# Optimization experiments

Hardware: AMD Instinct MI355X
Metric: run time of the kernel (lower is better)

The kernel has to match this reference:

```python
import jax, jax.numpy as jnp
import numpy as np

HEADS = 16


def setup_inputs() -> dict:
    key = jax.random.key(0)
    ks = jax.random.split(key, 6)
    B, S, D = 2, 2048, 1024
    return {
        "x": jax.random.normal(ks[0], (B, S, D), dtype=jnp.float32),
        "q_in": jax.random.normal(ks[1], (B, S, D), dtype=jnp.float32),
        "WQ": jax.random.normal(ks[2], (D, D), dtype=jnp.float32) * 0.03,
        "WK": jax.random.normal(ks[3], (D, D), dtype=jnp.float32) * 0.03,
        "WV": jax.random.normal(ks[4], (D, D), dtype=jnp.float32) * 0.03,
        "WO": jax.random.normal(ks[5], (D, D), dtype=jnp.float32) * 0.03,
    }


def reference(x, q_in, WQ, WK, WV, WO):
    B, S, D = x.shape
    H = HEADS
    hd = D // H
    # projections; tf.split on last dim == reshape to (B,S,H,hd)
    Q = (q_in @ WQ).reshape(B, S, H, hd)
    K = (x @ WK).reshape(B, S, H, hd)
    V = (x @ WV).reshape(B, S, H, hd)
    scores = jnp.einsum("bqhd,bkhd->bhqk", Q, K)  # [B,H,S,S]
    # causal additive mask: 0 on/below diagonal, -inf above
    causal = jnp.tril(jnp.ones((S, S), dtype=bool))
    mask = jnp.where(causal, 0.0, -jnp.inf).astype(scores.dtype)
    # NOTE: original adds the mask BEFORE scaling, and scales by sqrt(d_model)
    attn = jax.nn.softmax((scores + mask) / np.sqrt(D).astype(scores.dtype), axis=-1)
    ctx = jnp.einsum("bhqk,bkhd->bqhd", attn, V).reshape(B, S, D)
    return ctx @ WO
```

## Files before the change

kernel.cpp:

```cpp
#include <hip/hip_runtime.h>


typedef __bf16 bf16_t;
typedef __attribute__((ext_vector_type(8))) __bf16 bf16x8;
typedef __attribute__((ext_vector_type(4))) __bf16 bf16x4;
typedef __attribute__((ext_vector_type(4))) float f32x4;

#define SCALE_LOG2E 0.045084220027780106f
#define FIXED_MAX 8.0f

__device__ __forceinline__ void async_load16(const void* g, void* l) {
  __builtin_amdgcn_global_load_lds(
      (const __attribute__((address_space(1))) void*)g,
      (__attribute__((address_space(3))) void*)l, 16, 0, 0);
}

__global__ void prep(const float* __restrict__ x, const float* __restrict__ q,
                     const float* __restrict__ w0, const float* __restrict__ w1,
                     const float* __restrict__ w2, const float* __restrict__ w3,
                     bf16_t* __restrict__ xb, bf16_t* __restrict__ qb,
                     bf16_t* __restrict__ wt) {
  const int bid = blockIdx.x;
  if (bid < 4096) {
    const float* src = (bid >= 2048) ? q : x;
    bf16_t* dst = (bid >= 2048) ? qb : xb;
    const size_t i = ((size_t)(bid & 2047) * 256 + threadIdx.x) * 8;
    float4 v0 = *(const float4*)(src + i);
    float4 v1 = *(const float4*)(src + i + 4);
    bf16x8 o;
    o[0] = (bf16_t)v0.x; o[1] = (bf16_t)v0.y; o[2] = (bf16_t)v0.z; o[3] = (bf16_t)v0.w;
    o[4] = (bf16_t)v1.x; o[5] = (bf16_t)v1.y; o[6] = (bf16_t)v1.z; o[7] = (bf16_t)v1.w;
    *(bf16x8*)(dst + i) = o;
  } else {
    const int wb = bid - 4096;
    const int z = wb >> 8;
    const float* W = z == 0 ? w0 : z == 1 ? w1 : z == 2 ? w2 : w3;
    bf16_t* dst = wt + (size_t)z * 1048576;
    const int r0 = ((wb >> 4) & 15) * 64, c0 = (wb & 15) * 64;
    __shared__ bf16_t t[64][72];
#pragma unroll
    for (int i = 0; i < 16; ++i) {
      int flat = i * 256 + threadIdx.x;
      int r = flat >> 6, c = flat & 63;
      t[c][r] = (bf16_t)W[(size_t)(r0 + r) * 1024 + c0 + c];
    }
    __syncthreads();
    const int c = threadIdx.x >> 2, seg = (threadIdx.x & 3) * 16;
    bf16x8 a = *(const bf16x8*)&t[c][seg];
    bf16x8 b = *(const bf16x8*)&t[c][seg + 8];
    bf16_t* drow = dst + (size_t)(c0 + c) * 1024 + r0 + seg;
    *(bf16x8*)drow = a;
    *(bf16x8*)(drow + 8) = b;
  }
}

template <int MODE>
__global__ __launch_bounds__(256, MODE == 2 ? 4 : 2) void gemm128(
    const bf16_t* __restrict__ Aq, const bf16_t* __restrict__ Ax,
    const bf16_t* __restrict__ Bt,
    bf16_t* __restrict__ Cq, bf16_t* __restrict__ Cvt, float* __restrict__ Cf) {
  constexpr int K = 1024;
  constexpr int NT = (MODE == 2) ? 2 : 4;
  constexpr int NROWS = NT * 32;
  const int n0 = blockIdx.x * NROWS;
  const int m0 = blockIdx.y * 128;
  const bf16_t* A = (MODE == 0 && n0 >= 1024) ? Ax : Aq;

  __shared__ bf16_t lA[128 * 32];
  __shared__ bf16_t lB[NROWS * 32];

  const int tid = threadIdx.x;
  const int w = tid >> 6, l = tid & 63;
  const int wm = (w & 1) * 64, wn = (w >> 1) * (NT * 16);
  const int sr = l >> 2;
  const int sk = (l & 3) * 8;
  const int fr = l & 15, fc = (l >> 4) * 8;

  f32x4 acc[4][NT] = {};

  for (int kt = 0; kt < K; kt += 32) {
    __syncthreads();
#pragma unroll
    for (int c = 0; c < 2; ++c) {
      const int ch = w * 2 + c;
      async_load16(A + (size_t)(m0 + ch * 16 + sr) * K + kt + sk, &lA[ch * 512]);
      if (NT == 4 || c == 0) {
        const int bch = (NT == 4) ? ch : w;
        async_load16(Bt + (size_t)(n0 + bch * 16 + sr) * K + kt + sk, &lB[bch * 512]);
      }
    }
    __syncthreads();
    bf16x8 af[4], bfr[NT];
#pragma unroll
    for (int i = 0; i < 4; ++i) af[i] = *(const bf16x8*)&lA[(wm + i * 16 + fr) * 32 + fc];
#pragma unroll
    for (int j = 0; j < NT; ++j) bfr[j] = *(const bf16x8*)&lB[(wn + j * 16 + fr) * 32 + fc];
#pragma unroll
    for (int i = 0; i < 4; ++i)
#pragma unroll
      for (int j = 0; j < NT; ++j)
        acc[i][j] = __builtin_amdgcn_mfma_f32_16x16x32_bf16(af[i], bfr[j], acc[i][j], 0, 0, 0);
  }

  if (MODE == 2) {
#pragma unroll
    for (int i = 0; i < 4; ++i) {
      const int m = m0 + wm + i * 16 + (l >> 4) * 4;
#pragma unroll
      for (int j = 0; j < NT; ++j) {
        const int n = n0 + wn + j * 16 + fr;
#pragma unroll
        for (int r = 0; r < 4; ++r) Cf[(size_t)(m + r) * 1024 + n] = acc[i][j][r];
      }
    }
  } else if (n0 < 2048) {
#pragma unroll
    for (int i = 0; i < 4; ++i) {
      const int m = m0 + wm + i * 16 + (l >> 4) * 4;
#pragma unroll
      for (int j = 0; j < NT; ++j) {
        const int n = n0 + wn + j * 16 + fr;
#pragma unroll
        for (int r = 0; r < 4; ++r) Cq[(size_t)(m + r) * 3072 + n] = (bf16_t)acc[i][j][r];
      }
    }
  } else {
#pragma unroll
    for (int i = 0; i < 4; ++i) {
      const int mb = m0 + wm + i * 16 + (l >> 4) * 4;
      const int bb = mb >> 11, ss = mb & 2047;
#pragma unroll
      for (int j = 0; j < NT; ++j) {
        const int nn = n0 - 2048 + wn + j * 16 + fr;
        const int hh = nn >> 6, dd = nn & 63;
        bf16x4 pk;
#pragma unroll
        for (int r = 0; r < 4; ++r) pk[r] = (bf16_t)acc[i][j][r];
        *(bf16x4*)(Cvt + (size_t)((bb * 16 + hh) * 64 + dd) * 2048 + ss) = pk;
      }
    }
  }
}

__global__ __launch_bounds__(256, 2) void attn128(const bf16_t* __restrict__ qkv,
                                                  const bf16_t* __restrict__ vt,
                                                  bf16_t* __restrict__ ctx) {
  const int y = blockIdx.y;
  const int qt = (y < 8) ? (15 - y) : (y - 8);
  const int bh = blockIdx.x;
  const int b = bh >> 4, h = bh & 15;
  const int tid = threadIdx.x, w = tid >> 6, l = tid & 63;
  const int fr = l & 15, fq = l >> 4;

  __shared__ __align__(16) bf16_t lK[2][64 * 64];
  __shared__ __align__(16) bf16_t lV[2][64 * 64];
  __shared__ __align__(16) bf16_t lP[4][32 * 72];

  const int q0 = qt * 128 + w * 32;

  bf16x8 qf[2][2];
#pragma unroll
  for (int u = 0; u < 2; ++u)
#pragma unroll
    for (int ks = 0; ks < 2; ++ks)
      qf[u][ks] = *(const bf16x8*)(qkv + (size_t)(b * 2048 + q0 + u * 16 + fr) * 3072 +
                                   h * 64 + ks * 32 + fq * 8);

  bf16x8 ones;
#pragma unroll
  for (int i = 0; i < 8; ++i) ones[i] = (bf16_t)1.0f;

  f32x4 o[2][4] = {};
  f32x4 liacc[2] = {};

  const int srow = l >> 3;
  const int swz = ((l & 7) ^ srow) * 8;
  const int xr = fr & 7;

  const int ktmax = 2 * qt + 1;
  const bf16_t* kg = qkv + (size_t)b * 2048 * 3072 + 1024 + h * 64;
  const bf16_t* vg = vt + (size_t)(b * 16 + h) * 64 * 2048;

#pragma unroll
  for (int c = 0; c < 2; ++c) {
    const int row = w * 16 + c * 8 + srow;
    async_load16(kg + (size_t)row * 3072 + swz, &lK[0][(w * 16 + c * 8) * 64]);
    async_load16(vg + (size_t)row * 2048 + swz, &lV[0][(w * 16 + c * 8) * 64]);
  }

  for (int kt = 0; kt <= ktmax; ++kt) {
    const int buf = kt & 1;
    __syncthreads();
    if (kt < ktmax) {
#pragma unroll
      for (int c = 0; c < 2; ++c) {
        const int row = w * 16 + c * 8 + srow;
        async_load16(kg + (size_t)((kt + 1) * 64 + row) * 3072 + swz,
                     &lK[buf ^ 1][(w * 16 + c * 8) * 64]);
        async_load16(vg + (size_t)row * 2048 + (kt + 1) * 64 + swz,
                     &lV[buf ^ 1][(w * 16 + c * 8) * 64]);
      }
    }

    const int kbase = kt * 64;
    if (kbase > q0 + 31) continue;

    f32x4 s[2][4] = {};
#pragma unroll
    for (int t = 0; t < 4; ++t)
#pragma unroll
      for (int ks = 0; ks < 2; ++ks) {
        bf16x8 kf = *(const bf16x8*)&lK[buf][(t * 16 + fr) * 64 + ((ks * 4 + fq) ^ xr) * 8];
        s[0][t] = __builtin_amdgcn_mfma_f32_16x16x32_bf16(kf, qf[0][ks], s[0][t], 0, 0, 0);
        s[1][t] = __builtin_amdgcn_mfma_f32_16x16x32_bf16(kf, qf[1][ks], s[1][t], 0, 0, 0);
      }

#pragma unroll
    for (int u = 0; u < 2; ++u) {
      const int qq = q0 + u * 16 + fr;
      const bool needmask = (kbase + 63) > (q0 + u * 16);
#pragma unroll
      for (int t = 0; t < 4; ++t) {
        bf16x4 pk;
#pragma unroll
        for (int r = 0; r < 4; ++r) {
          float v = fmaf(s[u][t][r], SCALE_LOG2E, -FIXED_MAX);
          if (needmask && (kbase + t * 16 + fq * 4 + r > qq)) v = -1e30f;
          pk[r] = (bf16_t)__builtin_amdgcn_exp2f(v);
        }
        *(bf16x4*)&lP[w][(u * 16 + fr) * 72 + t * 16 + fq * 4] = pk;
      }
    }

    bf16x8 pf[2][2];
#pragma unroll
    for (int u = 0; u < 2; ++u)
#pragma unroll
      for (int g = 0; g < 2; ++g)
        pf[u][g] = *(const bf16x8*)&lP[w][(u * 16 + fr) * 72 + g * 32 + fq * 8];
#pragma unroll
    for (int g = 0; g < 2; ++g) {
#pragma unroll
      for (int dt = 0; dt < 4; ++dt) {
        bf16x8 vf = *(const bf16x8*)&lV[buf][(dt * 16 + fr) * 64 + ((g * 4 + fq) ^ xr) * 8];
        o[0][dt] = __builtin_amdgcn_mfma_f32_16x16x32_bf16(vf, pf[0][g], o[0][dt], 0, 0, 0);
        o[1][dt] = __builtin_amdgcn_mfma_f32_16x16x32_bf16(vf, pf[1][g], o[1][dt], 0, 0, 0);
      }
      liacc[0] = __builtin_amdgcn_mfma_f32_16x16x32_bf16(ones, pf[0][g], liacc[0], 0, 0, 0);
      liacc[1] = __builtin_amdgcn_mfma_f32_16x16x32_bf16(ones, pf[1][g], liacc[1], 0, 0, 0);
    }
  }

#pragma unroll
  for (int u = 0; u < 2; ++u) {
    const float inv = 1.f / liacc[u][0];
    bf16_t* cb = ctx + (size_t)(b * 2048 + q0 + u * 16 + fr) * 1024 + h * 64;
#pragma unroll
    for (int dt = 0; dt < 4; ++dt) {
      bf16x4 ov;
#pragma unroll
      for (int r = 0; r < 4; ++r) ov[r] = (bf16_t)(o[u][dt][r] * inv);
      *(bf16x4*)(cb + dt * 16 + fq * 4) = ov;
    }
  }
}

extern "C" void kernel_launch(void* const* d_in, const int* in_sizes, int n_in,
                              void* d_out, int out_size, void* d_ws, size_t ws_size,
                              hipStream_t stream) {
  const float* x  = (const float*)d_in[0];
  const float* q  = (const float*)d_in[1];
  const float* WQ = (const float*)d_in[2];
  const float* WK = (const float*)d_in[3];
  const float* WV = (const float*)d_in[4];
  const float* WO = (const float*)d_in[5];
  float* out = (float*)d_out;

  bf16_t* qb  = (bf16_t*)d_ws;
  bf16_t* xb  = qb + 4194304;
  bf16_t* wt  = xb + 4194304;
  bf16_t* qkv = wt + 4194304;
  bf16_t* vtp = qkv + (size_t)4096 * 3072;
  bf16_t* ctx = vtp + 4194304;

  prep<<<dim3(5120), 256, 0, stream>>>(x, q, WQ, WK, WV, WO, xb, qb, wt);
  gemm128<0><<<dim3(24, 32), 256, 0, stream>>>(qb, xb, wt, qkv, vtp, nullptr);
  attn128<<<dim3(32, 16), 256, 0, stream>>>(qkv, vtp, ctx);
  gemm128<2><<<dim3(16, 32), 256, 0, stream>>>(ctx, ctx, wt + (size_t)3072 * 1024,
                                               nullptr, nullptr, out);
}
```

Measured before the change: 200.6 us.

## Pair complementary 64-row query tiles per block for balanced causal attention

Each attention block now processes two 64-row query tiles in sequence, one late (16+p) and one early (15-p), so every block does roughly the same total causal work. Before, each block handled a single 128-row tile, reordered to launch heavy tiles first. Each wave now holds 16 query rows instead of 32, which lowers register pressure but halves MFMA reuse of each K/V fragment loaded from LDS. K/V tiles are reloaded for the second phase, and the per-kt skip check is removed.

```diff
diff --git a/kernel.cpp b/kernel.cpp
--- a/kernel.cpp
+++ b/kernel.cpp
@@ -142,11 +142,10 @@
   }
 }
 
-__global__ __launch_bounds__(256, 2) void attn128(const bf16_t* __restrict__ qkv,
+__global__ __launch_bounds__(256, 2) void attn64p(const bf16_t* __restrict__ qkv,
                                                   const bf16_t* __restrict__ vt,
                                                   bf16_t* __restrict__ ctx) {
-  const int y = blockIdx.y;
-  const int qt = (y < 8) ? (15 - y) : (y - 8);
+  const int p = blockIdx.y;
   const int bh = blockIdx.x;
   const int b = bh >> 4, h = bh & 15;
   const int tid = threadIdx.x, w = tid >> 6, l = tid & 63;
@@ -154,112 +153,103 @@
 
   __shared__ __align__(16) bf16_t lK[2][64 * 64];
   __shared__ __align__(16) bf16_t lV[2][64 * 64];
-  __shared__ __align__(16) bf16_t lP[4][32 * 72];
-
-  const int q0 = qt * 128 + w * 32;
-
-  bf16x8 qf[2][2];
-#pragma unroll
-  for (int u = 0; u < 2; ++u)
-#pragma unroll
-    for (int ks = 0; ks < 2; ++ks)
-      qf[u][ks] = *(const bf16x8*)(qkv + (size_t)(b * 2048 + q0 + u * 16 + fr) * 3072 +
-                                   h * 64 + ks * 32 + fq * 8);
-
-  bf16x8 ones;
-#pragma unroll
-  for (int i = 0; i < 8; ++i) ones[i] = (bf16_t)1.0f;
-
-  f32x4 o[2][4] = {};
-  f32x4 liacc[2] = {};
+  __shared__ __align__(16) bf16_t lP[4][16 * 72];
+
+  const bf16_t* kg = qkv + (size_t)b * 2048 * 3072 + 1024 + h * 64;
+  const bf16_t* vg = vt + (size_t)(b * 16 + h) * 64 * 2048;
 
   const int srow = l >> 3;
   const int swz = ((l & 7) ^ srow) * 8;
   const int xr = fr & 7;
 
-  const int ktmax = 2 * qt + 1;
-  const bf16_t* kg = qkv + (size_t)b * 2048 * 3072 + 1024 + h * 64;
-  const bf16_t* vg = vt + (size_t)(b * 16 + h) * 64 * 2048;
-
-#pragma unroll
-  for (int c = 0; c < 2; ++c) {
-    const int row = w * 16 + c * 8 + srow;
-    async_load16(kg + (size_t)row * 3072 + swz, &lK[0][(w * 16 + c * 8) * 64]);
-    async_load16(vg + (size_t)row * 2048 + swz, &lV[0][(w * 16 + c * 8) * 64]);
-  }
-
-  for (int kt = 0; kt <= ktmax; ++kt) {
-    const int buf = kt & 1;
-    __syncthreads();
-    if (kt < ktmax) {
-#pragma unroll
-      for (int c = 0; c < 2; ++c) {
-        const int row = w * 16 + c * 8 + srow;
-        async_load16(kg + (size_t)((kt + 1) * 64 + row) * 3072 + swz,
-                     &lK[buf ^ 1][(w * 16 + c * 8) * 64]);
-        async_load16(vg + (size_t)row * 2048 + (kt + 1) * 64 + swz,
-                     &lV[buf ^ 1][(w * 16 + c * 8) * 64]);
-      }
-    }
-
-    const int kbase = kt * 64;
-    if (kbase > q0 + 31) continue;
-
-    f32x4 s[2][4] = {};
-#pragma unroll
-    for (int t = 0; t < 4; ++t)
-#pragma unroll
-      for (int ks = 0; ks < 2; ++ks) {
-        bf16x8 kf = *(const bf16x8*)&lK[buf][(t * 16 + fr) * 64 + ((ks * 4 + fq) ^ xr) * 8];
-        s[0][t] = __builtin_amdgcn_mfma_f32_16x16x32_bf16(kf, qf[0][ks], s[0][t], 0, 0, 0);
-        s[1][t] = __builtin_amdgcn_mfma_f32_16x16x32_bf16(kf, qf[1][ks], s[1][t], 0, 0, 0);
-      }
-
-#pragma unroll
-    for (int u = 0; u < 2; ++u) {
-      const int qq = q0 + u * 16 + fr;
-      const bool needmask = (kbase + 63) > (q0 + u * 16);
+  bf16x8 ones;
+#pragma unroll
+  for (int i = 0; i < 8; ++i) ones[i] = (bf16_t)1.0f;
+
+#pragma unroll 1
+  for (int phase = 0; phase < 2; ++phase) {
+    const int qt = (phase == 0) ? (16 + p) : (15 - p);
+    const int q0 = qt * 64;
+    const int qw = q0 + w * 16;
+    const int ktmax = qt;
+
+    bf16x8 qf[2];
+#pragma unroll
+    for (int ks = 0; ks < 2; ++ks)
+      qf[ks] = *(const bf16x8*)(qkv + (size_t)(b * 2048 + qw + fr) * 3072 +
+                                h * 64 + ks * 32 + fq * 8);
+
+    f32x4 o[4] = {};
+    f32x4 liacc = {};
+
+    if (phase == 1) __syncthreads();
+#pragma unroll
+    for (int c = 0; c < 2; ++c) {
+      const int row = w * 16 + c * 8 + srow;
+      async_load16(kg + (size_t)row * 3072 + swz, &lK[0][(w * 16 + c * 8) * 64]);
+      async_load16(vg + (size_t)row * 2048 + swz, &lV[0][(w * 16 + c * 8) * 64]);
+    }
+
+    for (int kt = 0; kt <= ktmax; ++kt) {
+      const int buf = kt & 1;
+      __syncthreads();
+      if (kt < ktmax) {
+#pragma unroll
+        for (int c = 0; c < 2; ++c) {
+          const int row = w * 16 + c * 8 + srow;
+          async_load16(kg + (size_t)((kt + 1) * 64 + row) * 3072 + swz,
+                       &lK[buf ^ 1][(w * 16 + c * 8) * 64]);
+          async_load16(vg + (size_t)row * 2048 + (kt + 1) * 64 + swz,
+                       &lV[buf ^ 1][(w * 16 + c * 8) * 64]);
+        }
+      }
+
+      f32x4 s[4] = {};
+#pragma unroll
+      for (int t = 0; t < 4; ++t)
+#pragma unroll
+        for (int ks = 0; ks < 2; ++ks) {
+          bf16x8 kf = *(const bf16x8*)&lK[buf][(t * 16 + fr) * 64 + ((ks * 4 + fq) ^ xr) * 8];
+          s[t] = __builtin_amdgcn_mfma_f32_16x16x32_bf16(kf, qf[ks], s[t], 0, 0, 0);
+        }
+
+      const int kbase = kt * 64;
+      const int qq = qw + fr;
+      const bool needmask = (kbase + 63) > qw;
 #pragma unroll
       for (int t = 0; t < 4; ++t) {
         bf16x4 pk;
 #pragma unroll
         for (int r = 0; r < 4; ++r) {
-          float v = fmaf(s[u][t][r], SCALE_LOG2E, -FIXED_MAX);
+          float v = fmaf(s[t][r], SCALE_LOG2E, -FIXED_MAX);
           if (needmask && (kbase + t * 16 + fq * 4 + r > qq)) v = -1e30f;
           pk[r] = (bf16_t)__builtin_amdgcn_exp2f(v);
         }
-        *(bf16x4*)&lP[w][(u * 16 + fr) * 72 + t * 16 + fq * 4] = pk;
-      }
-    }
-
-    bf16x8 pf[2][2];
-#pragma unroll
-    for (int u = 0; u < 2; ++u)
+        *(bf16x4*)&lP[w][fr * 72 + t * 16 + fq * 4] = pk;
+      }
+
+      bf16x8 pf[2];
 #pragma unroll
       for (int g = 0; g < 2; ++g)
-        pf[u][g] = *(const bf16x8*)&lP[w][(u * 16 + fr) * 72 + g * 32 + fq * 8];
-#pragma unroll
-    for (int g = 0; g < 2; ++g) {
-#pragma unroll
-      for (int dt = 0; dt < 4; ++dt) {
-        bf16x8 vf = *(const bf16x8*)&lV[buf][(dt * 16 + fr) * 64 + ((g * 4 + fq) ^ xr) * 8];
-        o[0][dt] = __builtin_amdgcn_mfma_f32_16x16x32_bf16(vf, pf[0][g], o[0][dt], 0, 0, 0);
-        o[1][dt] = __builtin_amdgcn_mfma_f32_16x16x32_bf16(vf, pf[1][g], o[1][dt], 0, 0, 0);
-      }
-      liacc[0] = __builtin_amdgcn_mfma_f32_16x16x32_bf16(ones, pf[0][g], liacc[0], 0, 0, 0);
-      liacc[1] = __builtin_amdgcn_mfma_f32_16x16x32_bf16(ones, pf[1][g], liacc[1], 0, 0, 0);
-    }
-  }
-
-#pragma unroll
-  for (int u = 0; u < 2; ++u) {
-    const float inv = 1.f / liacc[u][0];
-    bf16_t* cb = ctx + (size_t)(b * 2048 + q0 + u * 16 + fr) * 1024 + h * 64;
+        pf[g] = *(const bf16x8*)&lP[w][fr * 72 + g * 32 + fq * 8];
+#pragma unroll
+      for (int g = 0; g < 2; ++g) {
+#pragma unroll
+        for (int dt = 0; dt < 4; ++dt) {
+          bf16x8 vf = *(const bf16x8*)&lV[buf][(dt * 16 + fr) * 64 + ((g * 4 + fq) ^ xr) * 8];
+          o[dt] = __builtin_amdgcn_mfma_f32_16x16x32_bf16(vf, pf[g], o[dt], 0, 0, 0);
+        }
+        liacc = __builtin_amdgcn_mfma_f32_16x16x32_bf16(ones, pf[g], liacc, 0, 0, 0);
+      }
+    }
+
+    const float inv = 1.f / liacc[0];
+    bf16_t* cb = ctx + (size_t)(b * 2048 + qw + fr) * 1024 + h * 64;
 #pragma unroll
     for (int dt = 0; dt < 4; ++dt) {
       bf16x4 ov;
 #pragma unroll
-      for (int r = 0; r < 4; ++r) ov[r] = (bf16_t)(o[u][dt][r] * inv);
+      for (int r = 0; r < 4; ++r) ov[r] = (bf16_t)(o[dt][r] * inv);
       *(bf16x4*)(cb + dt * 16 + fq * 4) = ov;
     }
   }
@@ -285,7 +275,7 @@
 
   prep<<<dim3(5120), 256, 0, stream>>>(x, q, WQ, WK, WV, WO, xb, qb, wt);
   gemm128<0><<<dim3(24, 32), 256, 0, stream>>>(qb, xb, wt, qkv, vtp, nullptr);
-  attn128<<<dim3(32, 16), 256, 0, stream>>>(qkv, vtp, ctx);
+  attn64p<<<dim3(32, 16), 256, 0, stream>>>(qkv, vtp, ctx);
   gemm128<2><<<dim3(16, 32), 256, 0, stream>>>(ctx, ctx, wt + (size_t)3072 * 1024,
                                                nullptr, nullptr, out);
 }
```

Result: faster. 193.6 us (-3.5%).

## Split attention key tiles across wave pairs and pair causal query tiles per block

Applied to the files above, without the earlier changes.

Each block now processes two 64-row query tiles in sequence (tile 16+p, then tile 15-p), so every block does the same amount of causal work. Within a tile, the four waves split into two query halves and two key halves. Each wave handles 32 keys per step, and the two key halves are combined through an LDS reduction before the output is written. The aim is to balance causal load across blocks and reduce the per-wave key work, at the cost of extra syncs, added LDS for the reduction, and reloading K/V for the second phase.

```diff
diff --git a/kernel.cpp b/kernel.cpp
--- a/kernel.cpp
+++ b/kernel.cpp
@@ -142,125 +142,145 @@
   }
 }
 
-__global__ __launch_bounds__(256, 2) void attn128(const bf16_t* __restrict__ qkv,
+__global__ __launch_bounds__(256, 2) void attn64k(const bf16_t* __restrict__ qkv,
                                                   const bf16_t* __restrict__ vt,
                                                   bf16_t* __restrict__ ctx) {
-  const int y = blockIdx.y;
-  const int qt = (y < 8) ? (15 - y) : (y - 8);
+  const int p = blockIdx.y;
   const int bh = blockIdx.x;
   const int b = bh >> 4, h = bh & 15;
   const int tid = threadIdx.x, w = tid >> 6, l = tid & 63;
   const int fr = l & 15, fq = l >> 4;
+  const int qhalf = w & 1, khalf = w >> 1;
 
   __shared__ __align__(16) bf16_t lK[2][64 * 64];
   __shared__ __align__(16) bf16_t lV[2][64 * 64];
-  __shared__ __align__(16) bf16_t lP[4][32 * 72];
-
-  const int q0 = qt * 128 + w * 32;
-
-  bf16x8 qf[2][2];
-#pragma unroll
-  for (int u = 0; u < 2; ++u)
-#pragma unroll
-    for (int ks = 0; ks < 2; ++ks)
-      qf[u][ks] = *(const bf16x8*)(qkv + (size_t)(b * 2048 + q0 + u * 16 + fr) * 3072 +
-                                   h * 64 + ks * 32 + fq * 8);
-
-  bf16x8 ones;
-#pragma unroll
-  for (int i = 0; i < 8; ++i) ones[i] = (bf16_t)1.0f;
-
-  f32x4 o[2][4] = {};
-  f32x4 liacc[2] = {};
+  __shared__ __align__(16) bf16_t lP[4][32 * 32];
+  __shared__ __align__(16) float lRed[2][32][68];
+
+  const bf16_t* kg = qkv + (size_t)b * 2048 * 3072 + 1024 + h * 64;
+  const bf16_t* vg = vt + (size_t)(b * 16 + h) * 64 * 2048;
 
   const int srow = l >> 3;
   const int swz = ((l & 7) ^ srow) * 8;
   const int xr = fr & 7;
-
-  const int ktmax = 2 * qt + 1;
-  const bf16_t* kg = qkv + (size_t)b * 2048 * 3072 + 1024 + h * 64;
-  const bf16_t* vg = vt + (size_t)(b * 16 + h) * 64 * 2048;
-
-#pragma unroll
-  for (int c = 0; c < 2; ++c) {
-    const int row = w * 16 + c * 8 + srow;
-    async_load16(kg + (size_t)row * 3072 + swz, &lK[0][(w * 16 + c * 8) * 64]);
-    async_load16(vg + (size_t)row * 2048 + swz, &lV[0][(w * 16 + c * 8) * 64]);
-  }
-
-  for (int kt = 0; kt <= ktmax; ++kt) {
-    const int buf = kt & 1;
-    __syncthreads();
-    if (kt < ktmax) {
-#pragma unroll
-      for (int c = 0; c < 2; ++c) {
-        const int row = w * 16 + c * 8 + srow;
-        async_load16(kg + (size_t)((kt + 1) * 64 + row) * 3072 + swz,
-                     &lK[buf ^ 1][(w * 16 + c * 8) * 64]);
-        async_load16(vg + (size_t)row * 2048 + (kt + 1) * 64 + swz,
-                     &lV[buf ^ 1][(w * 16 + c * 8) * 64]);
-      }
-    }
-
-    const int kbase = kt * 64;
-    if (kbase > q0 + 31) continue;
-
-    f32x4 s[2][4] = {};
-#pragma unroll
-    for (int t = 0; t < 4; ++t)
-#pragma unroll
-      for (int ks = 0; ks < 2; ++ks) {
-        bf16x8 kf = *(const bf16x8*)&lK[buf][(t * 16 + fr) * 64 + ((ks * 4 + fq) ^ xr) * 8];
-        s[0][t] = __builtin_amdgcn_mfma_f32_16x16x32_bf16(kf, qf[0][ks], s[0][t], 0, 0, 0);
-        s[1][t] = __builtin_amdgcn_mfma_f32_16x16x32_bf16(kf, qf[1][ks], s[1][t], 0, 0, 0);
-      }
-
-#pragma unroll
-    for (int u = 0; u < 2; ++u) {
-      const int qq = q0 + u * 16 + fr;
-      const bool needmask = (kbase + 63) > (q0 + u * 16);
-#pragma unroll
-      for (int t = 0; t < 4; ++t) {
-        bf16x4 pk;
-#pragma unroll
-        for (int r = 0; r < 4; ++r) {
-          float v = fmaf(s[u][t][r], SCALE_LOG2E, -FIXED_MAX);
-          if (needmask && (kbase + t * 16 + fq * 4 + r > qq)) v = -1e30f;
-          pk[r] = (bf16_t)__builtin_amdgcn_exp2f(v);
+  const int fr3 = fr & 3;
+
+  bf16x8 ones;
+#pragma unroll
+  for (int i = 0; i < 8; ++i) ones[i] = (bf16_t)1.0f;
+
+#pragma unroll 1
+  for (int phase = 0; phase < 2; ++phase) {
+    const int qt = (phase == 0) ? (16 + p) : (15 - p);
+    const int q0 = qt * 64;
+    const int qw = q0 + qhalf * 32;
+
+    bf16x8 qf[2][2];
+#pragma unroll
+    for (int u = 0; u < 2; ++u)
+#pragma unroll
+      for (int ks = 0; ks < 2; ++ks)
+        qf[u][ks] = *(const bf16x8*)(qkv + (size_t)(b * 2048 + qw + u * 16 + fr) * 3072 +
+                                     h * 64 + ks * 32 + fq * 8);
+
+    f32x4 o[2][4] = {};
+    f32x4 liacc[2] = {};
+
+    if (phase == 1) __syncthreads();
+#pragma unroll
+    for (int c = 0; c < 2; ++c) {
+      const int row = w * 16 + c * 8 + srow;
+      async_load16(kg + (size_t)row * 3072 + swz, &lK[0][(w * 16 + c * 8) * 64]);
+      async_load16(vg + (size_t)row * 2048 + swz, &lV[0][(w * 16 + c * 8) * 64]);
+    }
+
+    for (int kt = 0; kt <= qt; ++kt) {
+      const int buf = kt & 1;
+      __syncthreads();
+      if (kt < qt) {
+#pragma unroll
+        for (int c = 0; c < 2; ++c) {
+          const int row = w * 16 + c * 8 + srow;
+          async_load16(kg + (size_t)((kt + 1) * 64 + row) * 3072 + swz,
+                       &lK[buf ^ 1][(w * 16 + c * 8) * 64]);
+          async_load16(vg + (size_t)row * 2048 + (kt + 1) * 64 + swz,
+                       &lV[buf ^ 1][(w * 16 + c * 8) * 64]);
         }
-        *(bf16x4*)&lP[w][(u * 16 + fr) * 72 + t * 16 + fq * 4] = pk;
-      }
-    }
-
-    bf16x8 pf[2][2];
-#pragma unroll
-    for (int u = 0; u < 2; ++u)
-#pragma unroll
-      for (int g = 0; g < 2; ++g)
-        pf[u][g] = *(const bf16x8*)&lP[w][(u * 16 + fr) * 72 + g * 32 + fq * 8];
-#pragma unroll
-    for (int g = 0; g < 2; ++g) {
+      }
+
+      const int kb = kt * 64 + khalf * 32;
+      if (kb > qw + 31) continue;
+
+      f32x4 s[2][2] = {};
+#pragma unroll
+      for (int t = 0; t < 2; ++t)
+#pragma unroll
+        for (int ks = 0; ks < 2; ++ks) {
+          bf16x8 kf = *(const bf16x8*)&lK[buf][(khalf * 32 + t * 16 + fr) * 64 +
+                                              ((ks * 4 + fq) ^ xr) * 8];
+          s[0][t] = __builtin_amdgcn_mfma_f32_16x16x32_bf16(kf, qf[0][ks], s[0][t], 0, 0, 0);
+          s[1][t] = __builtin_amdgcn_mfma_f32_16x16x32_bf16(kf, qf[1][ks], s[1][t], 0, 0, 0);
+        }
+
+#pragma unroll
+      for (int u = 0; u < 2; ++u) {
+        const int qq = qw + u * 16 + fr;
+        const bool needmask = (kb + 31) > (qw + u * 16);
+#pragma unroll
+        for (int t = 0; t < 2; ++t) {
+          bf16x4 pk;
+#pragma unroll
+          for (int r = 0; r < 4; ++r) {
+            float v = fmaf(s[u][t][r], SCALE_LOG2E, -FIXED_MAX);
+            if (needmask && (kb + t * 16 + fq * 4 + r > qq)) v = -1e30f;
+            pk[r] = (bf16_t)__builtin_amdgcn_exp2f(v);
+          }
+          const int gs = (2 * t + (fq >> 1)) ^ fr3;
+          *(bf16x4*)&lP[w][(u * 16 + fr) * 32 + gs * 8 + (fq & 1) * 4] = pk;
+        }
+      }
+
+      bf16x8 pf[2];
+#pragma unroll
+      for (int u = 0; u < 2; ++u)
+        pf[u] = *(const bf16x8*)&lP[w][(u * 16 + fr) * 32 + (fq ^ fr3) * 8];
 #pragma unroll
       for (int dt = 0; dt < 4; ++dt) {
-        bf16x8 vf = *(const bf16x8*)&lV[buf][(dt * 16 + fr) * 64 + ((g * 4 + fq) ^ xr) * 8];
-        o[0][dt] = __builtin_amdgcn_mfma_f32_16x16x32_bf16(vf, pf[0][g], o[0][dt], 0, 0, 0);
-        o[1][dt] = __builtin_amdgcn_mfma_f32_16x16x32_bf16(vf, pf[1][g], o[1][dt], 0, 0, 0);
-      }
-      liacc[0] = __builtin_amdgcn_mfma_f32_16x16x32_bf16(ones, pf[0][g], liacc[0], 0, 0, 0);
-      liacc[1] = __builtin_amdgcn_mfma_f32_16x16x32_bf16(ones, pf[1][g], liacc[1], 0, 0, 0);
-    }
-  }
-
-#pragma unroll
-  for (int u = 0; u < 2; ++u) {
-    const float inv = 1.f / liacc[u][0];
-    bf16_t* cb = ctx + (size_t)(b * 2048 + q0 + u * 16 + fr) * 1024 + h * 64;
-#pragma unroll
-    for (int dt = 0; dt < 4; ++dt) {
-      bf16x4 ov;
-#pragma unroll
-      for (int r = 0; r < 4; ++r) ov[r] = (bf16_t)(o[u][dt][r] * inv);
-      *(bf16x4*)(cb + dt * 16 + fq * 4) = ov;
+        bf16x8 vf = *(const bf16x8*)&lV[buf][(dt * 16 + fr) * 64 +
+                                            ((khalf * 4 + fq) ^ xr) * 8];
+        o[0][dt] = __builtin_amdgcn_mfma_f32_16x16x32_bf16(vf, pf[0], o[0][dt], 0, 0, 0);
+        o[1][dt] = __builtin_amdgcn_mfma_f32_16x16x32_bf16(vf, pf[1], o[1][dt], 0, 0, 0);
+      }
+      liacc[0] = __builtin_amdgcn_mfma_f32_16x16x32_bf16(ones, pf[0], liacc[0], 0, 0, 0);
+      liacc[1] = __builtin_amdgcn_mfma_f32_16x16x32_bf16(ones, pf[1], liacc[1], 0, 0, 0);
+    }
+
+    __syncthreads();
+    if (khalf) {
+#pragma unroll
+      for (int u = 0; u < 2; ++u) {
+#pragma unroll
+        for (int dt = 0; dt < 4; ++dt)
+          *(f32x4*)&lRed[qhalf][u * 16 + fr][dt * 16 + fq * 4] = o[u][dt];
+        if (fq == 0) lRed[qhalf][u * 16 + fr][64] = liacc[u][0];
+      }
+    }
+    __syncthreads();
+    if (!khalf) {
+#pragma unroll
+      for (int u = 0; u < 2; ++u) {
+        const float lsum = liacc[u][0] + lRed[qhalf][u * 16 + fr][64];
+        const float inv = 1.f / lsum;
+        bf16_t* cb = ctx + (size_t)(b * 2048 + qw + u * 16 + fr) * 1024 + h * 64;
+#pragma unroll
+        for (int dt = 0; dt < 4; ++dt) {
+          f32x4 v = o[u][dt] + *(f32x4*)&lRed[qhalf][u * 16 + fr][dt * 16 + fq * 4];
+          bf16x4 ov;
+#pragma unroll
+          for (int r = 0; r < 4; ++r) ov[r] = (bf16_t)(v[r] * inv);
+          *(bf16x4*)(cb + dt * 16 + fq * 4) = ov;
+        }
+      }
     }
   }
 }
@@ -285,7 +305,7 @@
 
   prep<<<dim3(5120), 256, 0, stream>>>(x, q, WQ, WK, WV, WO, xb, qb, wt);
   gemm128<0><<<dim3(24, 32), 256, 0, stream>>>(qb, xb, wt, qkv, vtp, nullptr);
-  attn128<<<dim3(32, 16), 256, 0, stream>>>(qkv, vtp, ctx);
+  attn64k<<<dim3(32, 16), 256, 0, stream>>>(qkv, vtp, ctx);
   gemm128<2><<<dim3(16, 32), 256, 0, stream>>>(ctx, ctx, wt + (size_t)3072 * 1024,
                                                nullptr, nullptr, out);
 }
```

Result: faster. 193.1 us (-3.7%).
